# Kernel tuning notes

Measured on AMD Instinct MI355X. Metric: run time of the kernel, lower is better.

The kernel has to match this reference:

```python
import jax, jax.numpy as jnp
import numpy as np

NQ = 12  # num_qubits
NL = 4   # num_layers (StronglyEntanglingLayers depth)
BATCH = 512


def _rx(a):
    # RX(a) = [[cos(a/2), -i sin(a/2)], [-i sin(a/2), cos(a/2)]]; a: (...,) float -> (...,2,2) complex64
    c = jnp.cos(a / 2)
    s = jnp.sin(a / 2)
    return jnp.stack([jnp.stack([c + 0j, -1j * s], -1),
                      jnp.stack([-1j * s, c + 0j], -1)], -2)


def _rot(phi, theta, omega):
    # Pennylane Rot(phi,theta,omega) = RZ(omega) RY(theta) RZ(phi)
    ct = jnp.cos(theta / 2)
    st = jnp.sin(theta / 2)
    ep = jnp.exp(-0.5j * (phi + omega))   # e^{-i(phi+omega)/2}
    em = jnp.exp(-0.5j * (phi - omega))   # e^{-i(phi-omega)/2}
    return jnp.stack([jnp.stack([ep * ct, -jnp.conj(em) * st], -1),
                      jnp.stack([em * st, jnp.conj(ep) * ct], -1)], -2)


def _apply_1q_shared(state, U, q):
    # state: (B,) + (2,)*n; U: (2,2) shared across batch
    s = jnp.moveaxis(state, q + 1, -1)
    s = s @ U.T
    return jnp.moveaxis(s, -1, q + 1)


def _apply_1q_batched(state, U, q):
    # U: (B,2,2), one gate per batch element (AngleEmbedding)
    s = jnp.moveaxis(state, q + 1, -1)
    s = jnp.einsum('b...i,bij->b...j', s, U)
    return jnp.moveaxis(s, -1, q + 1)


def _apply_cnot(state, c, t):
    # flip target axis on the control=1 slice
    s = jnp.moveaxis(state, (c + 1, t + 1), (1, 2))  # (B,2,2,rest)
    s = jnp.stack([s[:, 0], s[:, 1, ::-1]], axis=1)
    return jnp.moveaxis(s, (1, 2), (c + 1, t + 1))


def _circuit(batch_inputs, weights):
    B, n = batch_inputs.shape
    state = jnp.zeros((B, 2 ** n), jnp.complex64).at[:, 0].set(1.0)
    state = state.reshape((B,) + (2,) * n)
    # AngleEmbedding: RX(x_i) on wire i
    Ux = _rx(batch_inputs)  # (B,n,2,2)
    for q in range(n):
        state = _apply_1q_batched(state, Ux[:, q], q)
    # StronglyEntanglingLayers: per layer Rot on each wire then CNOT ring with range r
    Ur = _rot(weights[..., 0], weights[..., 1], weights[..., 2])  # (L,n,2,2)
    for l in range(NL):
        for q in range(n):
            state = _apply_1q_shared(state, Ur[l, q], q)
        r = (l % (n - 1)) + 1  # pennylane default ranges
        for q in range(n):
            state = _apply_cnot(state, q, (q + r) % n)
    # <Z_q> = p(0 on q) - p(1 on q)
    probs = state.real ** 2 + state.imag ** 2
    zs = []
    for q in range(n):
        p = jnp.moveaxis(probs, q + 1, 1).reshape(B, 2, -1).sum(-1)
        zs.append(p[:, 0] - p[:, 1])
    return jnp.stack(zs, axis=1)  # (B,n) float32


def setup_inputs() -> dict:
    key = jax.random.key(0)
    k1, k2, k3, k4 = jax.random.split(key, 4)
    return {
        'batch_inputs': jax.random.normal(k1, (BATCH, NQ), dtype=jnp.float32),
        'weights': jax.random.normal(k2, (NL, NQ, 3), dtype=jnp.float32),
        'head_w': jax.random.normal(k3, (1, NQ), dtype=jnp.float32) / np.sqrt(NQ),
        'head_b': jax.random.normal(k4, (1,), dtype=jnp.float32),
    }


def reference(batch_inputs, weights, head_w, head_b):
    expvals = _circuit(batch_inputs, weights)      # (B, NQ)
    return (expvals @ head_w.T + head_b)[:, 0]     # (B,)
```

## Files before the change

### kernel.cpp

```cpp
#include <hip/hip_runtime.h>

#define NQ 12
#define NL 4
#define NT 512

typedef float f32x2 __attribute__((ext_vector_type(2)));

constexpr unsigned sidx_c(unsigned x) { return x ^ ((x >> 4) & 14u) ^ ((x >> 8) & 14u); }

constexpr unsigned gmap_inv(int l, unsigned v) {
    int r = l + 1; unsigned x = v;
    for (int q = 0; q < NQ; ++q) {
        int cb = NQ - 1 - q, tw = (q + r) % NQ, tb = NQ - 1 - tw;
        x ^= ((x >> cb) & 1u) << tb;
    }
    return x;
}

struct Tabs {
    unsigned lcol[3][9];
    unsigned scol[3][8];
    unsigned rfin[NQ];
};
constexpr Tabs make_tabs() {
    Tabs T{};
    for (int l = 0; l < 3; ++l) {
        unsigned colb[12];
        for (int bit = 0; bit < 12; ++bit) colb[bit] = sidx_c(gmap_inv(l, 1u << bit)) << 3;
        for (int j = 0; j < 6; ++j) T.lcol[l][j] = colb[3 + j];
        T.lcol[l][6] = colb[9];
        T.lcol[l][7] = colb[10];
        T.lcol[l][8] = colb[11];
        for (int s = 0; s < 8; ++s) {
            unsigned v = 0;
            for (int bp = 0; bp < 3; ++bp) if ((s >> bp) & 1) v ^= colb[bp];
            T.scol[l][s] = v;
        }
    }
    for (int q = 0; q < NQ; ++q) {
        const int bpos = 11 - q;
        unsigned m = 0;
        for (int j = 0; j < 12; ++j)
            m |= ((gmap_inv(3, 1u << j) >> bpos) & 1u) << j;
        T.rfin[q] = m;
    }
    return T;
}
__constant__ Tabs TB = make_tabs();
constexpr Tabs CT = make_tabs();

template<int CTRL>
__device__ __forceinline__ f32x2 dpp2(f32x2 v) {
    f32x2 r;
    r.x = __int_as_float(__builtin_amdgcn_update_dpp(__float_as_int(v.x), __float_as_int(v.x), CTRL, 0xF, 0xF, false));
    r.y = __int_as_float(__builtin_amdgcn_update_dpp(__float_as_int(v.y), __float_as_int(v.y), CTRL, 0xF, 0xF, false));
    return r;
}
__device__ __forceinline__ void pswap32(f32x2 v, f32x2& lo, f32x2& hi) {
    float ax = v.x, bx = v.x;
    asm("v_permlane32_swap_b32 %0, %1" : "+v"(ax), "+v"(bx));
    float ay = v.y, by = v.y;
    asm("v_permlane32_swap_b32 %0, %1" : "+v"(ay), "+v"(by));
    lo = f32x2{ax, ay}; hi = f32x2{bx, by};
}
__device__ __forceinline__ void pswap16(f32x2 v, f32x2& ev, f32x2& od) {
    float ax = v.x, bx = v.x;
    asm("v_permlane16_swap_b32 %0, %1" : "+v"(ax), "+v"(bx));
    float ay = v.y, by = v.y;
    asm("v_permlane16_swap_b32 %0, %1" : "+v"(ay), "+v"(by));
    ev = f32x2{ax, ay}; od = f32x2{bx, by};
}

__device__ __forceinline__ void gates3to11(f32x2 rp[4], f32x2 ip[4], const float (*gmL)[8], int lane) {
    {
        const float4 ga = *(const float4*)&gmL[3][0];
        const float4 gb = *(const float4*)&gmL[3][4];
        const int h = (lane >> 5) & 1;
        const float car = h ? gb.x : ga.x, cai = h ? gb.y : ga.y;
        const float cbr = h ? gb.z : ga.z, cbi = h ? gb.w : ga.w;
        #pragma unroll
        for (int k = 0; k < 4; ++k) {
            f32x2 r0r, r1r, r0i, r1i;
            pswap32(rp[k], r0r, r1r);
            pswap32(ip[k], r0i, r1i);
            rp[k] = car*r0r - cai*r0i + cbr*r1r - cbi*r1i;
            ip[k] = cai*r0r + car*r0i + cbi*r1r + cbr*r1i;
        }
    }
    {
        const float4 ga = *(const float4*)&gmL[4][0];
        const float4 gb = *(const float4*)&gmL[4][4];
        const int h = (lane >> 4) & 1;
        const float car = h ? gb.x : ga.x, cai = h ? gb.y : ga.y;
        const float cbr = h ? gb.z : ga.z, cbi = h ? gb.w : ga.w;
        #pragma unroll
        for (int k = 0; k < 4; ++k) {
            f32x2 r0r, r1r, r0i, r1i;
            pswap16(rp[k], r0r, r1r);
            pswap16(ip[k], r0i, r1i);
            rp[k] = car*r0r - cai*r0i + cbr*r1r - cbi*r1i;
            ip[k] = cai*r0r + car*r0i + cbi*r1r + cbr*r1i;
        }
    }
    {
        const float4 ga = *(const float4*)&gmL[5][0];
        const float4 gb = *(const float4*)&gmL[5][4];
        const int h = (lane >> 3) & 1;
        const float cMer = h ? gb.z : ga.x, cMei = h ? gb.w : ga.y;
        const float cOtr = h ? gb.x : ga.z, cOti = h ? gb.y : ga.w;
        #pragma unroll
        for (int k = 0; k < 4; ++k) {
            const f32x2 pR = dpp2<0x128>(rp[k]), pI = dpp2<0x128>(ip[k]);
            const f32x2 nr = cMer*rp[k] - cMei*ip[k] + cOtr*pR - cOti*pI;
            const f32x2 ni = cMei*rp[k] + cMer*ip[k] + cOti*pR + cOtr*pI;
            rp[k] = nr; ip[k] = ni;
        }
    }
    {
        const float4 ga = *(const float4*)&gmL[6][0];
        const float4 gb = *(const float4*)&gmL[6][4];
        const int h = (lane >> 2) & 1;
        const float cMer = h ? gb.z : ga.x, cMei = h ? gb.w : ga.y;
        const float cOtr = h ? gb.x : ga.z, cOti = h ? gb.y : ga.w;
        #pragma unroll
        for (int k = 0; k < 4; ++k) {
            const f32x2 pR = dpp2<0xB1>(dpp2<0x4E>(dpp2<0x141>(rp[k])));
            const f32x2 pI = dpp2<0xB1>(dpp2<0x4E>(dpp2<0x141>(ip[k])));
            const f32x2 nr = cMer*rp[k] - cMei*ip[k] + cOtr*pR - cOti*pI;
            const f32x2 ni = cMei*rp[k] + cMer*ip[k] + cOti*pR + cOtr*pI;
            rp[k] = nr; ip[k] = ni;
        }
    }
    {
        const float4 ga = *(const float4*)&gmL[7][0];
        const float4 gb = *(const float4*)&gmL[7][4];
        const int h = (lane >> 1) & 1;
        const float cMer = h ? gb.z : ga.x, cMei = h ? gb.w : ga.y;
        const float cOtr = h ? gb.x : ga.z, cOti = h ? gb.y : ga.w;
        #pragma unroll
        for (int k = 0; k < 4; ++k) {
            const f32x2 pR = dpp2<0x4E>(rp[k]), pI = dpp2<0x4E>(ip[k]);
            const f32x2 nr = cMer*rp[k] - cMei*ip[k] + cOtr*pR - cOti*pI;
            const f32x2 ni = cMei*rp[k] + cMer*ip[k] + cOti*pR + cOtr*pI;
            rp[k] = nr; ip[k] = ni;
        }
    }
    {
        const float4 ga = *(const float4*)&gmL[8][0];
        const float4 gb = *(const float4*)&gmL[8][4];
        const int h = lane & 1;
        const float cMer = h ? gb.z : ga.x, cMei = h ? gb.w : ga.y;
        const float cOtr = h ? gb.x : ga.z, cOti = h ? gb.y : ga.w;
        #pragma unroll
        for (int k = 0; k < 4; ++k) {
            const f32x2 pR = dpp2<0xB1>(rp[k]), pI = dpp2<0xB1>(ip[k]);
            const f32x2 nr = cMer*rp[k] - cMei*ip[k] + cOtr*pR - cOti*pI;
            const f32x2 ni = cMei*rp[k] + cMer*ip[k] + cOti*pR + cOtr*pI;
            rp[k] = nr; ip[k] = ni;
        }
    }
    {
        const float4 ga = *(const float4*)&gmL[9][0];
        const float4 gb = *(const float4*)&gmL[9][4];
        #pragma unroll
        for (int h2 = 0; h2 < 2; ++h2) {
            const int k0 = h2, k1 = h2 + 2;
            const f32x2 a0r = rp[k0], a0i = ip[k0], a1r = rp[k1], a1i = ip[k1];
            rp[k0] = ga.x*a0r - ga.y*a0i + ga.z*a1r - ga.w*a1i;
            ip[k0] = ga.y*a0r + ga.x*a0i + ga.w*a1r + ga.z*a1i;
            rp[k1] = gb.x*a0r - gb.y*a0i + gb.z*a1r - gb.w*a1i;
            ip[k1] = gb.y*a0r + gb.x*a0i + gb.w*a1r + gb.z*a1i;
        }
    }
    {
        const float4 ga = *(const float4*)&gmL[10][0];
        const float4 gb = *(const float4*)&gmL[10][4];
        #pragma unroll
        for (int h2 = 0; h2 < 2; ++h2) {
            const int k0 = 2 * h2, k1 = k0 + 1;
            const f32x2 a0r = rp[k0], a0i = ip[k0], a1r = rp[k1], a1i = ip[k1];
            rp[k0] = ga.x*a0r - ga.y*a0i + ga.z*a1r - ga.w*a1i;
            ip[k0] = ga.y*a0r + ga.x*a0i + ga.w*a1r + ga.z*a1i;
            rp[k1] = gb.x*a0r - gb.y*a0i + gb.z*a1r - gb.w*a1i;
            ip[k1] = gb.y*a0r + gb.x*a0i + gb.w*a1r + gb.z*a1i;
        }
    }
    {
        const float4 ga = *(const float4*)&gmL[11][0];
        const float4 gb = *(const float4*)&gmL[11][4];
        const f32x2 K0r = f32x2{ga.x, gb.x}, K0i = f32x2{ga.y, gb.y};
        const f32x2 K1r = f32x2{ga.z, gb.z}, K1i = f32x2{ga.w, gb.w};
        #pragma unroll
        for (int k = 0; k < 4; ++k) {
            const float a0r = rp[k].x, a0i = ip[k].x, a1r = rp[k].y, a1i = ip[k].y;
            rp[k] = K0r*a0r - K0i*a0i + K1r*a1r - K1i*a1i;
            ip[k] = K0i*a0r + K0r*a0i + K1i*a1r + K1r*a1i;
        }
    }
}

__device__ __forceinline__ void read_w012(f32x2 rp[4], f32x2 ip[4], const float2* st, unsigned wbyte,
                                          const float (*gmL)[8], int b11, int b10, int b9) {
    const float* G0 = gmL[0];
    const float* G1 = gmL[1];
    const float* G2 = gmL[2];
    const float a0r = G0[6*b11],   a0i = G0[6*b11+1];
    const float q0r = G0[2*b11+2], q0i = G0[2*b11+3];
    const float a1r = G1[6*b10],   a1i = G1[6*b10+1];
    const float q1r = G1[2*b10+2], q1i = G1[2*b10+3];
    const float a2r = G2[6*b9],    a2i = G2[6*b9+1];
    const float q2r = G2[2*b9+2],  q2i = G2[2*b9+3];
    const float m00r = a0r*a1r - a0i*a1i, m00i = a0r*a1i + a0i*a1r;
    const float m01r = a0r*q1r - a0i*q1i, m01i = a0r*q1i + a0i*q1r;
    const float m10r = q0r*a1r - q0i*a1i, m10i = q0r*a1i + q0i*a1r;
    const float m11r = q0r*q1r - q0i*q1i, m11i = q0r*q1i + q0i*q1r;
    float cr[8], ci[8];
    cr[0] = m00r*a2r - m00i*a2i; ci[0] = m00r*a2i + m00i*a2r;
    cr[1] = m00r*q2r - m00i*q2i; ci[1] = m00r*q2i + m00i*q2r;
    cr[2] = m01r*a2r - m01i*a2i; ci[2] = m01r*a2i + m01i*a2r;
    cr[3] = m01r*q2r - m01i*q2i; ci[3] = m01r*q2i + m01i*q2r;
    cr[4] = m10r*a2r - m10i*a2i; ci[4] = m10r*a2i + m10i*a2r;
    cr[5] = m10r*q2r - m10i*q2i; ci[5] = m10r*q2i + m10i*q2r;
    cr[6] = m11r*a2r - m11i*a2i; ci[6] = m11r*a2i + m11i*a2r;
    cr[7] = m11r*q2r - m11i*q2i; ci[7] = m11r*q2i + m11i*q2r;
    #pragma unroll
    for (int k = 0; k < 4; ++k) {
        const unsigned base = wbyte ^ ((unsigned)k << 4);
        f32x2 rr = f32x2{0.f, 0.f}, ii = f32x2{0.f, 0.f};
        #pragma unroll
        for (int o = 0; o < 8; ++o) {
            const float4 v = *(const float4*)((const char*)st + (base ^ ((unsigned)o * 0x1010u)));
            const f32x2 sr = f32x2{v.x, v.z}, si = f32x2{v.y, v.w};
            rr += cr[o]*sr - ci[o]*si;
            ii += ci[o]*sr + cr[o]*si;
        }
        rp[k] = rr; ip[k] = ii;
    }
}

__device__ __forceinline__ void scatter_l(const f32x2 rp[4], const f32x2 ip[4], float2* st,
                                          int l, int lane, int b9, int b10, int b11) {
    unsigned sbase = 0;
    #pragma unroll
    for (int j = 0; j < 6; ++j) if ((lane >> j) & 1) sbase ^= TB.lcol[l][j];
    if (b9)  sbase ^= TB.lcol[l][6];
    if (b10) sbase ^= TB.lcol[l][7];
    if (b11) sbase ^= TB.lcol[l][8];
    #pragma unroll
    for (int k = 0; k < 4; ++k) {
        *(float2*)((char*)st + (sbase ^ TB.scol[l][2 * k]))     = make_float2(rp[k].x, ip[k].x);
        *(float2*)((char*)st + (sbase ^ TB.scol[l][2 * k + 1])) = make_float2(rp[k].y, ip[k].y);
    }
}

__global__ __launch_bounds__(NT) void qsim_kernel(
    const float* __restrict__ xin,
    const float* __restrict__ wts,
    const float* __restrict__ hw,
    const float* __restrict__ hb,
    float* __restrict__ out)
{
    __shared__ alignas(16) float2 st[4096];
    __shared__ float gm[NL * NQ][8];
    __shared__ float wred[8];

    const int tid  = threadIdx.x;
    const int lane = tid & 63;
    const int wv   = tid >> 6;
    const int b    = blockIdx.x;
    const int b11 = wv >> 2, b10 = (wv >> 1) & 1, b9 = wv & 1;

    if (tid < NL * NQ) {
        const float phi = wts[tid * 3 + 0];
        const float th  = wts[tid * 3 + 1];
        const float om  = wts[tid * 3 + 2];
        const float ct  = cosf(0.5f * th), stt = sinf(0.5f * th);
        const float apo = -0.5f * (phi + om), amo = -0.5f * (phi - om);
        const float epr = cosf(apo), epi = sinf(apo);
        const float emr = cosf(amo), emi = sinf(amo);
        float* g = gm[tid];
        g[0] =  epr * ct;  g[1] =  epi * ct;
        g[2] = -emr * stt; g[3] =  emi * stt;
        g[4] =  emr * stt; g[5] =  emi * stt;
        g[6] =  epr * ct;  g[7] = -epi * ct;
    }

    float cv[NQ], sv[NQ];
    #pragma unroll
    for (int bp = 0; bp < NQ; ++bp) {
        const float a = 0.5f * xin[b * NQ + (NQ - 1 - bp)];
        cv[bp] = __cosf(a); sv[bp] = __sinf(a);
    }
    float MS[8];
    MS[0] = cv[0]; MS[1] = sv[0];
    #pragma unroll
    for (int bit = 1; bit < 3; ++bit) {
        #pragma unroll
        for (int j = (1 << bit) - 1; j >= 0; --j) {
            MS[j | (1 << bit)] = MS[j] * sv[bit];
            MS[j]              = MS[j] * cv[bit];
        }
    }

    const unsigned xb = ((unsigned)wv << 9) | ((unsigned)lane << 3);
    const unsigned wbyte = (xb ^ ((xb >> 4) & 14u) ^ ((xb >> 8) & 14u)) << 3;

    __syncthreads();

    f32x2 rp[4], ip[4];

    {
        const float* G0 = gm[0];
        const float* G1 = gm[1];
        const float* G2 = gm[2];
        const float w0r = G0[4*b11]*cv[11]   + G0[4*b11+3]*sv[11];
        const float w0i = G0[4*b11+1]*cv[11] - G0[4*b11+2]*sv[11];
        const float w1r = G1[4*b10]*cv[10]   + G1[4*b10+3]*sv[10];
        const float w1i = G1[4*b10+1]*cv[10] - G1[4*b10+2]*sv[10];
        const float w2r = G2[4*b9]*cv[9]     + G2[4*b9+3]*sv[9];
        const float w2i = G2[4*b9+1]*cv[9]   - G2[4*b9+2]*sv[9];
        const float t01r = w0r*w1r - w0i*w1i, t01i = w0r*w1i + w0i*w1r;
        float Ar = t01r*w2r - t01i*w2i;
        float Ai = t01r*w2i + t01i*w2r;
        float mm = 1.f;
        #pragma unroll
        for (int j = 0; j < 6; ++j) mm *= ((lane >> j) & 1) ? sv[3 + j] : cv[3 + j];
        Ar *= mm; Ai *= mm;
        const int pcl = __popc((unsigned)lane) & 3;
        float Br, Bi;
        if      (pcl == 0) { Br =  Ar; Bi =  Ai; }
        else if (pcl == 1) { Br =  Ai; Bi = -Ar; }
        else if (pcl == 2) { Br = -Ar; Bi = -Ai; }
        else               { Br = -Ai; Bi =  Ar; }
        #pragma unroll
        for (int s = 0; s < 8; ++s) {
            const float m = MS[s];
            const int pc = __builtin_popcount((unsigned)s) & 3;
            float ar, ai;
            if      (pc == 0) { ar =  Br*m; ai =  Bi*m; }
            else if (pc == 1) { ar =  Bi*m; ai = -Br*m; }
            else if (pc == 2) { ar = -Br*m; ai = -Bi*m; }
            else              { ar = -Bi*m; ai =  Br*m; }
            if (s & 1) { rp[s >> 1].y = ar; ip[s >> 1].y = ai; }
            else       { rp[s >> 1].x = ar; ip[s >> 1].x = ai; }
        }
        gates3to11(rp, ip, &gm[0], lane);
        scatter_l(rp, ip, st, 0, lane, b9, b10, b11);
    }
    __syncthreads();

    #pragma unroll
    for (int l = 1; l < NL; ++l) {
        read_w012(rp, ip, st, wbyte, &gm[l * NQ], b11, b10, b9);
        gates3to11(rp, ip, &gm[l * NQ], lane);
        if (l < 3) {
            __syncthreads();
            scatter_l(rp, ip, st, l, lane, b9, b10, b11);
            __syncthreads();
        }
    }

    {
        float CS[8];
        #pragma unroll
        for (int s = 0; s < 8; ++s) CS[s] = 0.f;
        #pragma unroll
        for (int q = 0; q < NQ; ++q) {
            const unsigned m = CT.rfin[q];
            const float wq = (__popc(xb & m) & 1) ? -hw[q] : hw[q];
            #pragma unroll
            for (int s = 0; s < 8; ++s)
                CS[s] += (__builtin_popcount((unsigned)s & m) & 1) ? -wq : wq;
        }
        f32x2 acc = f32x2{0.f, 0.f};
        #pragma unroll
        for (int k = 0; k < 4; ++k) {
            const f32x2 pr = rp[k]*rp[k] + ip[k]*ip[k];
            acc += pr * f32x2{CS[2 * k], CS[2 * k + 1]};
        }
        float sres = acc.x + acc.y;
        #pragma unroll
        for (int off = 32; off >= 1; off >>= 1)
            sres += __shfl_xor(sres, off, 64);
        if (lane == 0) wred[wv] = sres;
        __syncthreads();
        if (tid == 0) {
            float s = hb[0];
            #pragma unroll
            for (int w = 0; w < 8; ++w) s += wred[w];
            out[b] = s;
        }
    }
}

extern "C" void kernel_launch(void* const* d_in, const int* in_sizes, int n_in,
                              void* d_out, int out_size, void* d_ws, size_t ws_size,
                              hipStream_t stream) {
    const float* x  = (const float*)d_in[0];
    const float* wt = (const float*)d_in[1];
    const float* hw = (const float*)d_in[2];
    const float* hb = (const float*)d_in[3];
    float* outp = (float*)d_out;
    const int B = in_sizes[0] / NQ;
    qsim_kernel<<<B, NT, 0, stream>>>(x, wt, hw, hb, outp);
}
```

Baseline: 35.16 us.

## Defer three gates per layer into registers with permuted layouts and double-buffered LDS

Each layer's first three single-qubit gates were applied through an 8-way LDS gather in read_w012. They are replaced by gates deferred into registers, applied via lane exchanges (DPP or ds_swizzle) under per-stage qubit-position permutations chosen at compile time. The state moves through two ping-pong LDS buffers, so each layer transition needs one barrier instead of two, and each reload becomes a single float4 read per register pair. In exchange it doubles LDS use to 64 KB, adds more cross-lane shuffle work, and relies on complex compile-time layout tables that are checked only by a static_assert.

```diff
diff --git a/kernel.cpp b/kernel.cpp
--- a/kernel.cpp
+++ b/kernel.cpp
@@ -6,9 +6,15 @@
 
 typedef float f32x2 __attribute__((ext_vector_type(2)));
 
-constexpr unsigned sidx_c(unsigned x) { return x ^ ((x >> 4) & 14u) ^ ((x >> 8) & 14u); }
-
-constexpr unsigned gmap_inv(int l, unsigned v) {
+constexpr unsigned gmap_f(int l, unsigned v) {
+    int r = l + 1; unsigned x = v;
+    for (int q = NQ - 1; q >= 0; --q) {
+        int cb = NQ - 1 - q, tw = (q + r) % NQ, tb = NQ - 1 - tw;
+        x ^= ((x >> cb) & 1u) << tb;
+    }
+    return x;
+}
+constexpr unsigned ginv_f(int l, unsigned v) {
     int r = l + 1; unsigned x = v;
     for (int q = 0; q < NQ; ++q) {
         int cb = NQ - 1 - q, tw = (q + r) % NQ, tb = NQ - 1 - tw;
@@ -16,38 +22,67 @@
     }
     return x;
 }
+constexpr unsigned phi_f(unsigned x) { return x ^ ((x >> 4) & 14u) ^ ((x >> 8) & 14u); }
+
+constexpr int POS[5][12] = {
+    {0,1,2,3,4,5,6,7,8,9,10,11},
+    {9,10,11,0,1,2,3,4,5,6,7,8},
+    {0,1,2,9,5,6,10,7,8,11,3,4},
+    {0,4,5,1,6,7,2,8,9,3,10,11},
+    {0,9,2,4,1,10,3,5,11,6,7,8},
+};
+constexpr int DBITS[3][3] = { {0,1,2}, {3,6,9}, {8,10,11} };
+
+constexpr unsigned pv(int t, unsigned v) { unsigned r = 0; for (int b = 0; b < 12; ++b) if ((v >> b) & 1) r |= 1u << POS[t][b]; return r; }
+constexpr int bitat(int t, int i) { for (int b = 0; b < 12; ++b) if (POS[t][b] == i) return b; return -1; }
+constexpr unsigned rowmask(int l, int b) { unsigned r = 0; for (int j = 0; j < 12; ++j) if ((gmap_f(l, 1u << j) >> b) & 1) r |= 1u << j; return r; }
 
 struct Tabs {
-    unsigned lcol[3][9];
-    unsigned scol[3][8];
-    unsigned rfin[NQ];
+    unsigned lcol[4][9];
+    unsigned scol[4][8];
+    int      gq[4][9];
+    unsigned dm[3][3];
+    unsigned dr[3][3];
+    int      dg[3][3];
+    unsigned rfin[12];
 };
 constexpr Tabs make_tabs() {
     Tabs T{};
-    for (int l = 0; l < 3; ++l) {
-        unsigned colb[12];
-        for (int bit = 0; bit < 12; ++bit) colb[bit] = sidx_c(gmap_inv(l, 1u << bit)) << 3;
-        for (int j = 0; j < 6; ++j) T.lcol[l][j] = colb[3 + j];
-        T.lcol[l][6] = colb[9];
-        T.lcol[l][7] = colb[10];
-        T.lcol[l][8] = colb[11];
+    for (int t = 0; t <= 3; ++t) {
+        for (int i = 3; i < 12; ++i)
+            T.lcol[t][i - 3] = phi_f(pv(t + 1, ginv_f(t, 1u << bitat(t, i)))) << 3;
         for (int s = 0; s < 8; ++s) {
             unsigned v = 0;
-            for (int bp = 0; bp < 3; ++bp) if ((s >> bp) & 1) v ^= colb[bp];
-            T.scol[l][s] = v;
-        }
-    }
-    for (int q = 0; q < NQ; ++q) {
-        const int bpos = 11 - q;
-        unsigned m = 0;
-        for (int j = 0; j < 12; ++j)
-            m |= ((gmap_inv(3, 1u << j) >> bpos) & 1u) << j;
-        T.rfin[q] = m;
-    }
+            for (int bp = 0; bp < 3; ++bp)
+                if ((s >> bp) & 1) v ^= phi_f(pv(t + 1, ginv_f(t, 1u << bitat(t, bp)))) << 3;
+            T.scol[t][s] = v;
+        }
+        for (int i = 0; i < 9; ++i)
+            T.gq[t][i] = t * NQ + (11 - bitat(t, i));
+    }
+    for (int t = 2; t <= 4; ++t)
+        for (int j = 0; j < 3; ++j) {
+            const int b = DBITS[t - 2][j];
+            T.dm[t - 2][j] = pv(t, ginv_f(t - 1, 1u << b));
+            T.dr[t - 2][j] = pv(t, rowmask(t - 1, b));
+            T.dg[t - 2][j] = (t - 1) * NQ + (11 - b);
+        }
+    for (int q = 0; q < 12; ++q) T.rfin[q] = 1u << POS[4][11 - q];
     return T;
 }
-__constant__ Tabs TB = make_tabs();
 constexpr Tabs CT = make_tabs();
+
+constexpr bool chk() {
+    for (int t = 1; t <= 4; ++t) { unsigned seen = 0; for (int b = 0; b < 12; ++b) seen |= 1u << POS[t][b]; if (seen != 0xFFFu) return false; }
+    for (int t = 1; t <= 3; ++t)
+        for (int j = 0; j < 3; ++j) {
+            if (POS[t][DBITS[t - 1][j]] < 9) return false;
+            if (pv(t + 1, ginv_f(t, 1u << DBITS[t - 1][j])) >> 9) return false;
+        }
+    for (int j = 0; j < 3; ++j) if ((CT.dm[0][j] >> 3) > 31 || (CT.dm[1][j] >> 3) > 31 || (CT.dm[2][j] >> 3) > 31) return false;
+    return true;
+}
+static_assert(chk(), "layout constraints violated");
 
 template<int CTRL>
 __device__ __forceinline__ f32x2 dpp2(f32x2 v) {
@@ -70,11 +105,60 @@
     asm("v_permlane16_swap_b32 %0, %1" : "+v"(ay), "+v"(by));
     ev = f32x2{ax, ay}; od = f32x2{bx, by};
 }
-
-__device__ __forceinline__ void gates3to11(f32x2 rp[4], f32x2 ip[4], const float (*gmL)[8], int lane) {
-    {
-        const float4 ga = *(const float4*)&gmL[3][0];
-        const float4 gb = *(const float4*)&gmL[3][4];
+template<unsigned LAM>
+__device__ __forceinline__ f32x2 lexch(f32x2 v) {
+    static_assert(LAM < 32, "lane xor >=32 not needed");
+    if constexpr (LAM == 0) return v;
+    else if constexpr (LAM == 1) return dpp2<0xB1>(v);
+    else if constexpr (LAM == 2) return dpp2<0x4E>(v);
+    else if constexpr (LAM == 3) return dpp2<0x1B>(v);
+    else {
+        f32x2 r;
+        r.x = __int_as_float(__builtin_amdgcn_ds_swizzle(__float_as_int(v.x), (int)((LAM << 10) | 0x1F)));
+        r.y = __int_as_float(__builtin_amdgcn_ds_swizzle(__float_as_int(v.y), (int)((LAM << 10) | 0x1F)));
+        return r;
+    }
+}
+
+template<int DI, int J>
+__device__ __forceinline__ void deferred_gate(f32x2 rp[4], f32x2 ip[4], const float (*gm)[8], unsigned xbpos) {
+    constexpr unsigned m = CT.dm[DI][J];
+    constexpr unsigned r = CT.dr[DI][J];
+    constexpr unsigned lam = m >> 3;
+    constexpr unsigned s = m & 7u;
+    constexpr int gi = CT.dg[DI][J];
+    const float4 ga = *(const float4*)&gm[gi][0];
+    const float4 gb = *(const float4*)&gm[gi][4];
+    const int pt = __popc(xbpos & r) & 1;
+    const float oA_r = pt ? gb.z : ga.x, oA_i = pt ? gb.w : ga.y;
+    const float pA_r = pt ? gb.x : ga.z, pA_i = pt ? gb.y : ga.w;
+    const float oB_r = pt ? ga.x : gb.z, oB_i = pt ? ga.y : gb.w;
+    const float pB_r = pt ? ga.z : gb.x, pB_i = pt ? ga.w : gb.y;
+    f32x2 nr[4], ni[4];
+    #pragma unroll
+    for (int k = 0; k < 4; ++k) {
+        const int e0 = __builtin_popcount((unsigned)(2 * k) & (r & 7u)) & 1;
+        const int e1 = e0 ^ (int)(r & 1u);
+        const int ks = k ^ (int)(s >> 1);
+        f32x2 per = lexch<lam>(rp[ks]);
+        f32x2 pei = lexch<lam>(ip[ks]);
+        if (s & 1u) { per = f32x2{per.y, per.x}; pei = f32x2{pei.y, pei.x}; }
+        const f32x2 oR = f32x2{e0 ? oB_r : oA_r, e1 ? oB_r : oA_r};
+        const f32x2 oI = f32x2{e0 ? oB_i : oA_i, e1 ? oB_i : oA_i};
+        const f32x2 pR = f32x2{e0 ? pB_r : pA_r, e1 ? pB_r : pA_r};
+        const f32x2 pI = f32x2{e0 ? pB_i : pA_i, e1 ? pB_i : pA_i};
+        nr[k] = oR * rp[k] - oI * ip[k] + pR * per - pI * pei;
+        ni[k] = oI * rp[k] + oR * ip[k] + pI * per + pR * pei;
+    }
+    #pragma unroll
+    for (int k = 0; k < 4; ++k) { rp[k] = nr[k]; ip[k] = ni[k]; }
+}
+
+template<int P>
+__device__ __forceinline__ void gates9(f32x2 rp[4], f32x2 ip[4], const float (*gm)[8], int lane) {
+    {
+        const float4 ga = *(const float4*)&gm[CT.gq[P][8]][0];
+        const float4 gb = *(const float4*)&gm[CT.gq[P][8]][4];
         const int h = (lane >> 5) & 1;
         const float car = h ? gb.x : ga.x, cai = h ? gb.y : ga.y;
         const float cbr = h ? gb.z : ga.z, cbi = h ? gb.w : ga.w;
@@ -83,13 +167,13 @@
             f32x2 r0r, r1r, r0i, r1i;
             pswap32(rp[k], r0r, r1r);
             pswap32(ip[k], r0i, r1i);
-            rp[k] = car*r0r - cai*r0i + cbr*r1r - cbi*r1i;
-            ip[k] = cai*r0r + car*r0i + cbi*r1r + cbr*r1i;
-        }
-    }
-    {
-        const float4 ga = *(const float4*)&gmL[4][0];
-        const float4 gb = *(const float4*)&gmL[4][4];
+            rp[k] = car * r0r - cai * r0i + cbr * r1r - cbi * r1i;
+            ip[k] = cai * r0r + car * r0i + cbi * r1r + cbr * r1i;
+        }
+    }
+    {
+        const float4 ga = *(const float4*)&gm[CT.gq[P][7]][0];
+        const float4 gb = *(const float4*)&gm[CT.gq[P][7]][4];
         const int h = (lane >> 4) & 1;
         const float car = h ? gb.x : ga.x, cai = h ? gb.y : ga.y;
         const float cbr = h ? gb.z : ga.z, cbi = h ? gb.w : ga.w;
@@ -98,27 +182,27 @@
             f32x2 r0r, r1r, r0i, r1i;
             pswap16(rp[k], r0r, r1r);
             pswap16(ip[k], r0i, r1i);
-            rp[k] = car*r0r - cai*r0i + cbr*r1r - cbi*r1i;
-            ip[k] = cai*r0r + car*r0i + cbi*r1r + cbr*r1i;
-        }
-    }
-    {
-        const float4 ga = *(const float4*)&gmL[5][0];
-        const float4 gb = *(const float4*)&gmL[5][4];
+            rp[k] = car * r0r - cai * r0i + cbr * r1r - cbi * r1i;
+            ip[k] = cai * r0r + car * r0i + cbi * r1r + cbr * r1i;
+        }
+    }
+    {
+        const float4 ga = *(const float4*)&gm[CT.gq[P][6]][0];
+        const float4 gb = *(const float4*)&gm[CT.gq[P][6]][4];
         const int h = (lane >> 3) & 1;
         const float cMer = h ? gb.z : ga.x, cMei = h ? gb.w : ga.y;
         const float cOtr = h ? gb.x : ga.z, cOti = h ? gb.y : ga.w;
         #pragma unroll
         for (int k = 0; k < 4; ++k) {
             const f32x2 pR = dpp2<0x128>(rp[k]), pI = dpp2<0x128>(ip[k]);
-            const f32x2 nr = cMer*rp[k] - cMei*ip[k] + cOtr*pR - cOti*pI;
-            const f32x2 ni = cMei*rp[k] + cMer*ip[k] + cOti*pR + cOtr*pI;
+            const f32x2 nr = cMer * rp[k] - cMei * ip[k] + cOtr * pR - cOti * pI;
+            const f32x2 ni = cMei * rp[k] + cMer * ip[k] + cOti * pR + cOtr * pI;
             rp[k] = nr; ip[k] = ni;
         }
     }
     {
-        const float4 ga = *(const float4*)&gmL[6][0];
-        const float4 gb = *(const float4*)&gmL[6][4];
+        const float4 ga = *(const float4*)&gm[CT.gq[P][5]][0];
+        const float4 gb = *(const float4*)&gm[CT.gq[P][5]][4];
         const int h = (lane >> 2) & 1;
         const float cMer = h ? gb.z : ga.x, cMei = h ? gb.w : ga.y;
         const float cOtr = h ? gb.x : ga.z, cOti = h ? gb.y : ga.w;
@@ -126,141 +210,109 @@
         for (int k = 0; k < 4; ++k) {
             const f32x2 pR = dpp2<0xB1>(dpp2<0x4E>(dpp2<0x141>(rp[k])));
             const f32x2 pI = dpp2<0xB1>(dpp2<0x4E>(dpp2<0x141>(ip[k])));
-            const f32x2 nr = cMer*rp[k] - cMei*ip[k] + cOtr*pR - cOti*pI;
-            const f32x2 ni = cMei*rp[k] + cMer*ip[k] + cOti*pR + cOtr*pI;
+            const f32x2 nr = cMer * rp[k] - cMei * ip[k] + cOtr * pR - cOti * pI;
+            const f32x2 ni = cMei * rp[k] + cMer * ip[k] + cOti * pR + cOtr * pI;
             rp[k] = nr; ip[k] = ni;
         }
     }
     {
-        const float4 ga = *(const float4*)&gmL[7][0];
-        const float4 gb = *(const float4*)&gmL[7][4];
+        const float4 ga = *(const float4*)&gm[CT.gq[P][4]][0];
+        const float4 gb = *(const float4*)&gm[CT.gq[P][4]][4];
         const int h = (lane >> 1) & 1;
         const float cMer = h ? gb.z : ga.x, cMei = h ? gb.w : ga.y;
         const float cOtr = h ? gb.x : ga.z, cOti = h ? gb.y : ga.w;
         #pragma unroll
         for (int k = 0; k < 4; ++k) {
             const f32x2 pR = dpp2<0x4E>(rp[k]), pI = dpp2<0x4E>(ip[k]);
-            const f32x2 nr = cMer*rp[k] - cMei*ip[k] + cOtr*pR - cOti*pI;
-            const f32x2 ni = cMei*rp[k] + cMer*ip[k] + cOti*pR + cOtr*pI;
+            const f32x2 nr = cMer * rp[k] - cMei * ip[k] + cOtr * pR - cOti * pI;
+            const f32x2 ni = cMei * rp[k] + cMer * ip[k] + cOti * pR + cOtr * pI;
             rp[k] = nr; ip[k] = ni;
         }
     }
     {
-        const float4 ga = *(const float4*)&gmL[8][0];
-        const float4 gb = *(const float4*)&gmL[8][4];
+        const float4 ga = *(const float4*)&gm[CT.gq[P][3]][0];
+        const float4 gb = *(const float4*)&gm[CT.gq[P][3]][4];
         const int h = lane & 1;
         const float cMer = h ? gb.z : ga.x, cMei = h ? gb.w : ga.y;
         const float cOtr = h ? gb.x : ga.z, cOti = h ? gb.y : ga.w;
         #pragma unroll
         for (int k = 0; k < 4; ++k) {
             const f32x2 pR = dpp2<0xB1>(rp[k]), pI = dpp2<0xB1>(ip[k]);
-            const f32x2 nr = cMer*rp[k] - cMei*ip[k] + cOtr*pR - cOti*pI;
-            const f32x2 ni = cMei*rp[k] + cMer*ip[k] + cOti*pR + cOtr*pI;
+            const f32x2 nr = cMer * rp[k] - cMei * ip[k] + cOtr * pR - cOti * pI;
+            const f32x2 ni = cMei * rp[k] + cMer * ip[k] + cOti * pR + cOtr * pI;
             rp[k] = nr; ip[k] = ni;
         }
     }
     {
-        const float4 ga = *(const float4*)&gmL[9][0];
-        const float4 gb = *(const float4*)&gmL[9][4];
+        const float4 ga = *(const float4*)&gm[CT.gq[P][2]][0];
+        const float4 gb = *(const float4*)&gm[CT.gq[P][2]][4];
         #pragma unroll
         for (int h2 = 0; h2 < 2; ++h2) {
             const int k0 = h2, k1 = h2 + 2;
             const f32x2 a0r = rp[k0], a0i = ip[k0], a1r = rp[k1], a1i = ip[k1];
-            rp[k0] = ga.x*a0r - ga.y*a0i + ga.z*a1r - ga.w*a1i;
-            ip[k0] = ga.y*a0r + ga.x*a0i + ga.w*a1r + ga.z*a1i;
-            rp[k1] = gb.x*a0r - gb.y*a0i + gb.z*a1r - gb.w*a1i;
-            ip[k1] = gb.y*a0r + gb.x*a0i + gb.w*a1r + gb.z*a1i;
-        }
-    }
-    {
-        const float4 ga = *(const float4*)&gmL[10][0];
-        const float4 gb = *(const float4*)&gmL[10][4];
+            rp[k0] = ga.x * a0r - ga.y * a0i + ga.z * a1r - ga.w * a1i;
+            ip[k0] = ga.y * a0r + ga.x * a0i + ga.w * a1r + ga.z * a1i;
+            rp[k1] = gb.x * a0r - gb.y * a0i + gb.z * a1r - gb.w * a1i;
+            ip[k1] = gb.y * a0r + gb.x * a0i + gb.w * a1r + gb.z * a1i;
+        }
+    }
+    {
+        const float4 ga = *(const float4*)&gm[CT.gq[P][1]][0];
+        const float4 gb = *(const float4*)&gm[CT.gq[P][1]][4];
         #pragma unroll
         for (int h2 = 0; h2 < 2; ++h2) {
             const int k0 = 2 * h2, k1 = k0 + 1;
             const f32x2 a0r = rp[k0], a0i = ip[k0], a1r = rp[k1], a1i = ip[k1];
-            rp[k0] = ga.x*a0r - ga.y*a0i + ga.z*a1r - ga.w*a1i;
-            ip[k0] = ga.y*a0r + ga.x*a0i + ga.w*a1r + ga.z*a1i;
-            rp[k1] = gb.x*a0r - gb.y*a0i + gb.z*a1r - gb.w*a1i;
-            ip[k1] = gb.y*a0r + gb.x*a0i + gb.w*a1r + gb.z*a1i;
-        }
-    }
-    {
-        const float4 ga = *(const float4*)&gmL[11][0];
-        const float4 gb = *(const float4*)&gmL[11][4];
+            rp[k0] = ga.x * a0r - ga.y * a0i + ga.z * a1r - ga.w * a1i;
+            ip[k0] = ga.y * a0r + ga.x * a0i + ga.w * a1r + ga.z * a1i;
+            rp[k1] = gb.x * a0r - gb.y * a0i + gb.z * a1r - gb.w * a1i;
+            ip[k1] = gb.y * a0r + gb.x * a0i + gb.w * a1r + gb.z * a1i;
+        }
+    }
+    {
+        const float4 ga = *(const float4*)&gm[CT.gq[P][0]][0];
+        const float4 gb = *(const float4*)&gm[CT.gq[P][0]][4];
         const f32x2 K0r = f32x2{ga.x, gb.x}, K0i = f32x2{ga.y, gb.y};
         const f32x2 K1r = f32x2{ga.z, gb.z}, K1i = f32x2{ga.w, gb.w};
         #pragma unroll
         for (int k = 0; k < 4; ++k) {
             const float a0r = rp[k].x, a0i = ip[k].x, a1r = rp[k].y, a1i = ip[k].y;
-            rp[k] = K0r*a0r - K0i*a0i + K1r*a1r - K1i*a1i;
-            ip[k] = K0i*a0r + K0r*a0i + K1i*a1r + K1r*a1i;
-        }
-    }
-}
-
-__device__ __forceinline__ void read_w012(f32x2 rp[4], f32x2 ip[4], const float2* st, unsigned wbyte,
-                                          const float (*gmL)[8], int b11, int b10, int b9) {
-    const float* G0 = gmL[0];
-    const float* G1 = gmL[1];
-    const float* G2 = gmL[2];
-    const float a0r = G0[6*b11],   a0i = G0[6*b11+1];
-    const float q0r = G0[2*b11+2], q0i = G0[2*b11+3];
-    const float a1r = G1[6*b10],   a1i = G1[6*b10+1];
-    const float q1r = G1[2*b10+2], q1i = G1[2*b10+3];
-    const float a2r = G2[6*b9],    a2i = G2[6*b9+1];
-    const float q2r = G2[2*b9+2],  q2i = G2[2*b9+3];
-    const float m00r = a0r*a1r - a0i*a1i, m00i = a0r*a1i + a0i*a1r;
-    const float m01r = a0r*q1r - a0i*q1i, m01i = a0r*q1i + a0i*q1r;
-    const float m10r = q0r*a1r - q0i*a1i, m10i = q0r*a1i + q0i*a1r;
-    const float m11r = q0r*q1r - q0i*q1i, m11i = q0r*q1i + q0i*q1r;
-    float cr[8], ci[8];
-    cr[0] = m00r*a2r - m00i*a2i; ci[0] = m00r*a2i + m00i*a2r;
-    cr[1] = m00r*q2r - m00i*q2i; ci[1] = m00r*q2i + m00i*q2r;
-    cr[2] = m01r*a2r - m01i*a2i; ci[2] = m01r*a2i + m01i*a2r;
-    cr[3] = m01r*q2r - m01i*q2i; ci[3] = m01r*q2i + m01i*q2r;
-    cr[4] = m10r*a2r - m10i*a2i; ci[4] = m10r*a2i + m10i*a2r;
-    cr[5] = m10r*q2r - m10i*q2i; ci[5] = m10r*q2i + m10i*q2r;
-    cr[6] = m11r*a2r - m11i*a2i; ci[6] = m11r*a2i + m11i*a2r;
-    cr[7] = m11r*q2r - m11i*q2i; ci[7] = m11r*q2i + m11i*q2r;
+            rp[k] = K0r * a0r - K0i * a0i + K1r * a1r - K1i * a1i;
+            ip[k] = K0i * a0r + K0r * a0i + K1i * a1r + K1r * a1i;
+        }
+    }
+}
+
+template<int P>
+__device__ __forceinline__ void scatter_p(const f32x2 rp[4], const f32x2 ip[4], float2* wb, int lane, int wv) {
+    unsigned sbase = 0;
+    #pragma unroll
+    for (int j = 0; j < 6; ++j) if ((lane >> j) & 1) sbase ^= CT.lcol[P][j];
+    #pragma unroll
+    for (int j = 0; j < 3; ++j) if ((wv >> j) & 1) sbase ^= CT.lcol[P][6 + j];
     #pragma unroll
     for (int k = 0; k < 4; ++k) {
-        const unsigned base = wbyte ^ ((unsigned)k << 4);
-        f32x2 rr = f32x2{0.f, 0.f}, ii = f32x2{0.f, 0.f};
-        #pragma unroll
-        for (int o = 0; o < 8; ++o) {
-            const float4 v = *(const float4*)((const char*)st + (base ^ ((unsigned)o * 0x1010u)));
-            const f32x2 sr = f32x2{v.x, v.z}, si = f32x2{v.y, v.w};
-            rr += cr[o]*sr - ci[o]*si;
-            ii += ci[o]*sr + cr[o]*si;
-        }
-        rp[k] = rr; ip[k] = ii;
-    }
-}
-
-__device__ __forceinline__ void scatter_l(const f32x2 rp[4], const f32x2 ip[4], float2* st,
-                                          int l, int lane, int b9, int b10, int b11) {
-    unsigned sbase = 0;
-    #pragma unroll
-    for (int j = 0; j < 6; ++j) if ((lane >> j) & 1) sbase ^= TB.lcol[l][j];
-    if (b9)  sbase ^= TB.lcol[l][6];
-    if (b10) sbase ^= TB.lcol[l][7];
-    if (b11) sbase ^= TB.lcol[l][8];
+        *(float2*)((char*)wb + (sbase ^ CT.scol[P][2 * k]))     = make_float2(rp[k].x, ip[k].x);
+        *(float2*)((char*)wb + (sbase ^ CT.scol[P][2 * k + 1])) = make_float2(rp[k].y, ip[k].y);
+    }
+}
+
+__device__ __forceinline__ void readst(f32x2 rp[4], f32x2 ip[4], const float2* rb, unsigned wbyte) {
     #pragma unroll
     for (int k = 0; k < 4; ++k) {
-        *(float2*)((char*)st + (sbase ^ TB.scol[l][2 * k]))     = make_float2(rp[k].x, ip[k].x);
-        *(float2*)((char*)st + (sbase ^ TB.scol[l][2 * k + 1])) = make_float2(rp[k].y, ip[k].y);
-    }
-}
-
-__global__ __launch_bounds__(NT) void qsim_kernel(
+        const float4 v = *(const float4*)((const char*)rb + (wbyte ^ ((unsigned)k << 4)));
+        rp[k] = f32x2{v.x, v.z}; ip[k] = f32x2{v.y, v.w};
+    }
+}
+
+__global__ __launch_bounds__(NT, 4) void qsim_kernel(
     const float* __restrict__ xin,
     const float* __restrict__ wts,
     const float* __restrict__ hw,
     const float* __restrict__ hb,
     float* __restrict__ out)
 {
-    __shared__ alignas(16) float2 st[4096];
+    __shared__ alignas(16) float2 buf[2][4096];
     __shared__ float gm[NL * NQ][8];
     __shared__ float wred[8];
 
@@ -274,7 +326,7 @@
         const float phi = wts[tid * 3 + 0];
         const float th  = wts[tid * 3 + 1];
         const float om  = wts[tid * 3 + 2];
-        const float ct  = cosf(0.5f * th), stt = sinf(0.5f * th);
+        const float ct = cosf(0.5f * th), stt = sinf(0.5f * th);
         const float apo = -0.5f * (phi + om), amo = -0.5f * (phi - om);
         const float epr = cosf(apo), epi = sinf(apo);
         const float emr = cosf(amo), emi = sinf(amo);
@@ -302,8 +354,8 @@
         }
     }
 
-    const unsigned xb = ((unsigned)wv << 9) | ((unsigned)lane << 3);
-    const unsigned wbyte = (xb ^ ((xb >> 4) & 14u) ^ ((xb >> 8) & 14u)) << 3;
+    const unsigned xbpos = ((unsigned)wv << 9) | ((unsigned)lane << 3);
+    const unsigned wbyte = phi_f(xbpos) << 3;
 
     __syncthreads();
 
@@ -313,15 +365,15 @@
         const float* G0 = gm[0];
         const float* G1 = gm[1];
         const float* G2 = gm[2];
-        const float w0r = G0[4*b11]*cv[11]   + G0[4*b11+3]*sv[11];
-        const float w0i = G0[4*b11+1]*cv[11] - G0[4*b11+2]*sv[11];
-        const float w1r = G1[4*b10]*cv[10]   + G1[4*b10+3]*sv[10];
-        const float w1i = G1[4*b10+1]*cv[10] - G1[4*b10+2]*sv[10];
-        const float w2r = G2[4*b9]*cv[9]     + G2[4*b9+3]*sv[9];
-        const float w2i = G2[4*b9+1]*cv[9]   - G2[4*b9+2]*sv[9];
-        const float t01r = w0r*w1r - w0i*w1i, t01i = w0r*w1i + w0i*w1r;
-        float Ar = t01r*w2r - t01i*w2i;
-        float Ai = t01r*w2i + t01i*w2r;
+        const float w0r = G0[4 * b11] * cv[11]     + G0[4 * b11 + 3] * sv[11];
+        const float w0i = G0[4 * b11 + 1] * cv[11] - G0[4 * b11 + 2] * sv[11];
+        const float w1r = G1[4 * b10] * cv[10]     + G1[4 * b10 + 3] * sv[10];
+        const float w1i = G1[4 * b10 + 1] * cv[10] - G1[4 * b10 + 2] * sv[10];
+        const float w2r = G2[4 * b9] * cv[9]       + G2[4 * b9 + 3] * sv[9];
+        const float w2i = G2[4 * b9 + 1] * cv[9]   - G2[4 * b9 + 2] * sv[9];
+        const float t01r = w0r * w1r - w0i * w1i, t01i = w0r * w1i + w0i * w1r;
+        float Ar = t01r * w2r - t01i * w2i;
+        float Ai = t01r * w2i + t01i * w2r;
         float mm = 1.f;
         #pragma unroll
         for (int j = 0; j < 6; ++j) mm *= ((lane >> j) & 1) ? sv[3 + j] : cv[3 + j];
@@ -337,37 +389,52 @@
             const float m = MS[s];
             const int pc = __builtin_popcount((unsigned)s) & 3;
             float ar, ai;
-            if      (pc == 0) { ar =  Br*m; ai =  Bi*m; }
-            else if (pc == 1) { ar =  Bi*m; ai = -Br*m; }
-            else if (pc == 2) { ar = -Br*m; ai = -Bi*m; }
-            else              { ar = -Bi*m; ai =  Br*m; }
+            if      (pc == 0) { ar =  Br * m; ai =  Bi * m; }
+            else if (pc == 1) { ar =  Bi * m; ai = -Br * m; }
+            else if (pc == 2) { ar = -Br * m; ai = -Bi * m; }
+            else              { ar = -Bi * m; ai =  Br * m; }
             if (s & 1) { rp[s >> 1].y = ar; ip[s >> 1].y = ai; }
             else       { rp[s >> 1].x = ar; ip[s >> 1].x = ai; }
         }
-        gates3to11(rp, ip, &gm[0], lane);
-        scatter_l(rp, ip, st, 0, lane, b9, b10, b11);
+        gates9<0>(rp, ip, gm, lane);
+        scatter_p<0>(rp, ip, buf[0], lane, wv);
     }
     __syncthreads();
 
-    #pragma unroll
-    for (int l = 1; l < NL; ++l) {
-        read_w012(rp, ip, st, wbyte, &gm[l * NQ], b11, b10, b9);
-        gates3to11(rp, ip, &gm[l * NQ], lane);
-        if (l < 3) {
-            __syncthreads();
-            scatter_l(rp, ip, st, l, lane, b9, b10, b11);
-            __syncthreads();
-        }
-    }
-
-    {
+    readst(rp, ip, buf[0], wbyte);
+    gates9<1>(rp, ip, gm, lane);
+    scatter_p<1>(rp, ip, buf[1], lane, wv);
+    __syncthreads();
+
+    readst(rp, ip, buf[1], wbyte);
+    deferred_gate<0, 0>(rp, ip, gm, xbpos);
+    deferred_gate<0, 1>(rp, ip, gm, xbpos);
+    deferred_gate<0, 2>(rp, ip, gm, xbpos);
+    gates9<2>(rp, ip, gm, lane);
+    scatter_p<2>(rp, ip, buf[0], lane, wv);
+    __syncthreads();
+
+    readst(rp, ip, buf[0], wbyte);
+    deferred_gate<1, 0>(rp, ip, gm, xbpos);
+    deferred_gate<1, 1>(rp, ip, gm, xbpos);
+    deferred_gate<1, 2>(rp, ip, gm, xbpos);
+    gates9<3>(rp, ip, gm, lane);
+    scatter_p<3>(rp, ip, buf[1], lane, wv);
+    __syncthreads();
+
+    {
+        readst(rp, ip, buf[1], wbyte);
+        deferred_gate<2, 0>(rp, ip, gm, xbpos);
+        deferred_gate<2, 1>(rp, ip, gm, xbpos);
+        deferred_gate<2, 2>(rp, ip, gm, xbpos);
+
         float CS[8];
         #pragma unroll
         for (int s = 0; s < 8; ++s) CS[s] = 0.f;
         #pragma unroll
         for (int q = 0; q < NQ; ++q) {
             const unsigned m = CT.rfin[q];
-            const float wq = (__popc(xb & m) & 1) ? -hw[q] : hw[q];
+            const float wq = (__popc(xbpos & m) & 1) ? -hw[q] : hw[q];
             #pragma unroll
             for (int s = 0; s < 8; ++s)
                 CS[s] += (__builtin_popcount((unsigned)s & m) & 1) ? -wq : wq;
@@ -375,7 +442,7 @@
         f32x2 acc = f32x2{0.f, 0.f};
         #pragma unroll
         for (int k = 0; k < 4; ++k) {
-            const f32x2 pr = rp[k]*rp[k] + ip[k]*ip[k];
+            const f32x2 pr = rp[k] * rp[k] + ip[k] * ip[k];
             acc += pr * f32x2{CS[2 * k], CS[2 * k + 1]};
         }
         float sres = acc.x + acc.y;
```

After: 32.24 us. 8.3% less time.
